# Optimization experiments

Measured on AMD Instinct MI355X. Metric: run time of the kernel, lower is better.

The kernel has to match this reference:

```python
import jax, jax.numpy as jnp
import numpy as np

# GeoFormer.generate_proposal constants (cfg.threshold_ins, cfg.min_pts_num,
# instance classes start at semantic id 4 on ScanNet)
THRESHOLD = 0.5
MIN_PTS_NUM = 50
MIN_INST_CLASS = 4


def setup_inputs() -> dict:
    key = jax.random.key(0)
    k1, k2, k3, k4 = jax.random.split(key, 4)
    B, Q, N, C = 4, 128, 50000, 20
    mask_logits = jax.random.normal(k1, (B, Q, N), dtype=jnp.float32)
    cls_logits = jax.random.normal(k2, (B, Q, C), dtype=jnp.float32)
    seg_pred = jax.random.randint(k3, (B, N), 0, C, dtype=jnp.int64)
    fg_idxs = jax.random.randint(k4, (B * N,), 0, 300000, dtype=jnp.int64)
    return {"mask_logits": mask_logits, "cls_logits": cls_logits,
            "seg_pred": seg_pred, "fg_idxs": fg_idxs}


def reference(mask_logits, cls_logits, seg_pred, fg_idxs):
    # mask_logits: [B, Q, N]  per-query point-mask logits (dense form of the
    #   per-batch list in the original; batch_offsets become the B dim)
    # cls_logits:  [B, Q, C]  per-query class logits
    # seg_pred:    [B, N]     per-point semantic prediction
    # fg_idxs:     [B*N]      foreground -> original point id map
    B, Q, N = mask_logits.shape
    m = jax.nn.sigmoid(mask_logits)                         # [B, Q, N]
    cls_pred = jnp.argmax(cls_logits, axis=2)               # [B, Q]

    # (mask_logit_b[n] > threshold) & (seg_pred == cls_logits_pred[b, n])
    sel = (m > THRESHOLD) & (seg_pred[:, None, :] == cls_pred[:, :, None])  # [B,Q,N]
    cnt = sel.sum(axis=-1)                                  # [B, Q] proposal sizes

    # score = mean of sigmoid over selected points
    msel = jnp.where(sel, m, jnp.zeros((), m.dtype))
    scores = msel.sum(axis=-1) / jnp.maximum(cnt, 1).astype(m.dtype)  # [B, Q]

    # skip if too few points or a background/wall class (< 4)
    valid = (cnt >= MIN_PTS_NUM) & (cls_pred >= MIN_INST_CLASS)       # [B, Q]

    proposal_masks = sel & valid[:, :, None]                # dense proposal_idx
    scores = jnp.where(valid, scores, jnp.zeros((), scores.dtype))
    global_ids = fg_idxs.reshape(B, N)                      # fg_idxs remap per point
    return proposal_masks, scores, valid, cls_pred, global_ids
```

## Files before the change

kernel.cpp:

```cpp
#include <hip/hip_runtime.h>
#include <math.h>

#define BB 4
#define QQ 128
#define NN 50000
#define CC 20
#define ROWS (BB * QQ)
#define NV4 (NN / 4)
#define TPB 256
#define UNROLL 4
#define BPR 13
#define THRESH_CNT 50
#define MIN_CLS 4

typedef float f32x4 __attribute__((ext_vector_type(4)));
typedef int   i32x4 __attribute__((ext_vector_type(4)));

struct Ws {
    float sum[ROWS];
    int   cnt[ROWS];
    int   cls[ROWS];
    int   valid[ROWS];
};

__global__ void k0_argmax_zero(const float* __restrict__ cls_logits, Ws* ws) {
    int r = blockIdx.x * blockDim.x + threadIdx.x;
    if (r >= ROWS) return;
    const float* p = cls_logits + r * CC;
    float best = p[0];
    int bi = 0;
    #pragma unroll
    for (int c = 1; c < CC; ++c) {
        float v = p[c];
        if (v > best) { best = v; bi = c; }
    }
    ws->cls[r] = bi;
    ws->sum[r] = 0.0f;
    ws->cnt[r] = 0;
}

__global__ __launch_bounds__(256) void k1_select(
        const float* __restrict__ mask_logits,
        const int*   __restrict__ seg_pred,
        float* __restrict__ out_mask,
        Ws* __restrict__ ws) {
    const int row = blockIdx.y;
    const int b   = row >> 7;
    const int cls = ws->cls[row];

    const f32x4* __restrict__ ml = (const f32x4*)(mask_logits + (size_t)row * NN);
    const i32x4* __restrict__ sp = (const i32x4*)(seg_pred + b * NN);
    f32x4* __restrict__ om = (f32x4*)(out_mask + (size_t)row * NN);

    const int idx0 = blockIdx.x * (TPB * UNROLL) + threadIdx.x;

    f32x4 v[UNROLL];
    i32x4 s[UNROLL];
    bool  act[UNROLL];
    #pragma unroll
    for (int j = 0; j < UNROLL; ++j) {
        int idx = idx0 + j * TPB;
        act[j] = (idx < NV4);
        if (act[j]) {
            v[j] = ml[idx];
            s[j] = sp[idx];
        }
    }

    float lsum = 0.0f;
    int   lcnt = 0;
    #pragma unroll
    for (int j = 0; j < UNROLL; ++j) {
        if (!act[j]) continue;
        int idx = idx0 + j * TPB;
        f32x4 vv = v[j];
        i32x4 ss = s[j];
        bool s0 = (vv.x > 0.0f) & (ss.x == cls);
        bool s1 = (vv.y > 0.0f) & (ss.y == cls);
        bool s2 = (vv.z > 0.0f) & (ss.z == cls);
        bool s3 = (vv.w > 0.0f) & (ss.w == cls);
        float g0 = 1.0f / (1.0f + __expf(-vv.x));
        float g1 = 1.0f / (1.0f + __expf(-vv.y));
        float g2 = 1.0f / (1.0f + __expf(-vv.z));
        float g3 = 1.0f / (1.0f + __expf(-vv.w));
        f32x4 o;
        o.x = s0 ? 1.0f : 0.0f;
        o.y = s1 ? 1.0f : 0.0f;
        o.z = s2 ? 1.0f : 0.0f;
        o.w = s3 ? 1.0f : 0.0f;
        lsum += (s0 ? g0 : 0.0f) + (s1 ? g1 : 0.0f)
              + (s2 ? g2 : 0.0f) + (s3 ? g3 : 0.0f);
        lcnt += (int)s0 + (int)s1 + (int)s2 + (int)s3;
        __builtin_nontemporal_store(o, &om[idx]);
    }

    #pragma unroll
    for (int off = 32; off > 0; off >>= 1) {
        lsum += __shfl_down(lsum, off);
        lcnt += __shfl_down(lcnt, off);
    }
    __shared__ float ssum[4];
    __shared__ int   scnt[4];
    const int wave = threadIdx.x >> 6;
    const int lane = threadIdx.x & 63;
    if (lane == 0) { ssum[wave] = lsum; scnt[wave] = lcnt; }
    __syncthreads();
    if (threadIdx.x == 0) {
        float ts = ssum[0] + ssum[1] + ssum[2] + ssum[3];
        int   tc = scnt[0] + scnt[1] + scnt[2] + scnt[3];
        atomicAdd(&ws->sum[row], ts);
        atomicAdd(&ws->cnt[row], tc);
    }
}

__global__ void k2_finalize_gids(const int* __restrict__ fg,
                                 float* __restrict__ out,
                                 Ws* __restrict__ ws) {
    const int idx = blockIdx.x * blockDim.x + threadIdx.x;
    if (idx < ROWS) {
        int   cnt = ws->cnt[idx];
        int   cls = ws->cls[idx];
        float sum = ws->sum[idx];
        int valid = (cnt >= THRESH_CNT) && (cls >= MIN_CLS);
        ws->valid[idx] = valid;
        float* tail = out + (size_t)ROWS * NN;
        tail[idx]            = valid ? (sum / (float)max(cnt, 1)) : 0.0f;
        tail[ROWS + idx]     = valid ? 1.0f : 0.0f;
        tail[2 * ROWS + idx] = (float)cls;
    }
    const int nv4 = (BB * NN) / 4;
    if (idx < nv4) {
        float* gids = out + (size_t)ROWS * NN + 3 * ROWS;
        i32x4 v = ((const i32x4*)fg)[idx];
        f32x4 o;
        o.x = (float)v.x; o.y = (float)v.y; o.z = (float)v.z; o.w = (float)v.w;
        __builtin_nontemporal_store(o, &((f32x4*)gids)[idx]);
    }
}

__global__ __launch_bounds__(256) void k3_fixup(
        float* __restrict__ out_mask, const Ws* __restrict__ ws) {
    const int row = blockIdx.y;
    if (ws->valid[row]) return;
    f32x4* __restrict__ om = (f32x4*)(out_mask + (size_t)row * NN);
    const f32x4 z = {0.0f, 0.0f, 0.0f, 0.0f};
    const int idx0 = blockIdx.x * (TPB * UNROLL) + threadIdx.x;
    #pragma unroll
    for (int j = 0; j < UNROLL; ++j) {
        int idx = idx0 + j * TPB;
        if (idx < NV4) __builtin_nontemporal_store(z, &om[idx]);
    }
}

extern "C" void kernel_launch(void* const* d_in, const int* in_sizes, int n_in,
                              void* d_out, int out_size, void* d_ws, size_t ws_size,
                              hipStream_t stream) {
    const float* mask_logits = (const float*)d_in[0];
    const float* cls_logits  = (const float*)d_in[1];
    const int*   seg_pred    = (const int*)d_in[2];
    const int*   fg_idxs     = (const int*)d_in[3];

    float* out = (float*)d_out;
    Ws* ws = (Ws*)d_ws;

    float* out_mask = out;

    k0_argmax_zero<<<(ROWS + 255) / 256, 256, 0, stream>>>(cls_logits, ws);

    dim3 g1(BPR, ROWS);
    k1_select<<<g1, TPB, 0, stream>>>(mask_logits, seg_pred, out_mask, ws);

    const int gids_blocks = ((BB * NN) / 4 + 255) / 256;
    k2_finalize_gids<<<gids_blocks, 256, 0, stream>>>(fg_idxs, out, ws);

    k3_fixup<<<g1, TPB, 0, stream>>>(out_mask, ws);
}
```

Baseline: 197.8 us.

## Give each block a larger contiguous chunk with software-pipelined batched loads

Reduces blocks per row from 13 to 4. Each block now handles a contiguous quarter of the row (3125 float4s) as three batches of four loads plus a tail. The next batch is prefetched while the current one is computed, to hide memory latency and cut per-block launch and atomic overhead. The cost is fewer blocks in flight (2048 instead of 6656) and higher register pressure, which may lower occupancy for a bandwidth-bound kernel. The fixup kernel is changed to match the new partitioning.

```diff
diff --git a/kernel.cpp b/kernel.cpp
--- a/kernel.cpp
+++ b/kernel.cpp
@@ -8,8 +8,10 @@
 #define ROWS (BB * QQ)
 #define NV4 (NN / 4)
 #define TPB 256
-#define UNROLL 4
-#define BPR 13
+#define BPR 4
+#define QUOTA (NV4 / BPR)
+#define FULL_ITERS 12
+#define TAIL 53
 #define THRESH_CNT 50
 #define MIN_CLS 4
 
@@ -47,57 +49,89 @@
     const int row = blockIdx.y;
     const int b   = row >> 7;
     const int cls = ws->cls[row];
-
-    const f32x4* __restrict__ ml = (const f32x4*)(mask_logits + (size_t)row * NN);
-    const i32x4* __restrict__ sp = (const i32x4*)(seg_pred + b * NN);
-    f32x4* __restrict__ om = (f32x4*)(out_mask + (size_t)row * NN);
-
-    const int idx0 = blockIdx.x * (TPB * UNROLL) + threadIdx.x;
-
-    f32x4 v[UNROLL];
-    i32x4 s[UNROLL];
-    bool  act[UNROLL];
-    #pragma unroll
-    for (int j = 0; j < UNROLL; ++j) {
-        int idx = idx0 + j * TPB;
-        act[j] = (idx < NV4);
-        if (act[j]) {
-            v[j] = ml[idx];
-            s[j] = sp[idx];
-        }
-    }
+    const int off = blockIdx.x * QUOTA;
+
+    const f32x4* __restrict__ ml = (const f32x4*)(mask_logits + (size_t)row * NN) + off;
+    const i32x4* __restrict__ sp = (const i32x4*)(seg_pred + b * NN) + off;
+    f32x4* __restrict__ om = (f32x4*)(out_mask + (size_t)row * NN) + off;
+
+    const int t = threadIdx.x;
 
     float lsum = 0.0f;
     int   lcnt = 0;
-    #pragma unroll
-    for (int j = 0; j < UNROLL; ++j) {
-        if (!act[j]) continue;
-        int idx = idx0 + j * TPB;
-        f32x4 vv = v[j];
-        i32x4 ss = s[j];
-        bool s0 = (vv.x > 0.0f) & (ss.x == cls);
-        bool s1 = (vv.y > 0.0f) & (ss.y == cls);
-        bool s2 = (vv.z > 0.0f) & (ss.z == cls);
-        bool s3 = (vv.w > 0.0f) & (ss.w == cls);
+
+    f32x4 v0[4]; i32x4 s0v[4];
+    #pragma unroll
+    for (int j = 0; j < 4; ++j) {
+        v0[j]  = ml[t + j * TPB];
+        s0v[j] = sp[t + j * TPB];
+    }
+
+    #pragma unroll
+    for (int bat = 0; bat < 3; ++bat) {
+        f32x4 nv[4]; i32x4 ns[4];
+        if (bat < 2) {
+            const int nbase = (bat + 1) * (4 * TPB) + t;
+            #pragma unroll
+            for (int j = 0; j < 4; ++j) {
+                nv[j] = ml[nbase + j * TPB];
+                ns[j] = sp[nbase + j * TPB];
+            }
+        }
+        const int base = bat * (4 * TPB) + t;
+        #pragma unroll
+        for (int j = 0; j < 4; ++j) {
+            f32x4 vv = v0[j];
+            i32x4 ss = s0v[j];
+            bool c0 = (vv.x > 0.0f) & (ss.x == cls);
+            bool c1 = (vv.y > 0.0f) & (ss.y == cls);
+            bool c2 = (vv.z > 0.0f) & (ss.z == cls);
+            bool c3 = (vv.w > 0.0f) & (ss.w == cls);
+            float g0 = 1.0f / (1.0f + __expf(-vv.x));
+            float g1 = 1.0f / (1.0f + __expf(-vv.y));
+            float g2 = 1.0f / (1.0f + __expf(-vv.z));
+            float g3 = 1.0f / (1.0f + __expf(-vv.w));
+            f32x4 o;
+            o.x = c0 ? 1.0f : 0.0f;
+            o.y = c1 ? 1.0f : 0.0f;
+            o.z = c2 ? 1.0f : 0.0f;
+            o.w = c3 ? 1.0f : 0.0f;
+            lsum += (c0 ? g0 : 0.0f) + (c1 ? g1 : 0.0f)
+                  + (c2 ? g2 : 0.0f) + (c3 ? g3 : 0.0f);
+            lcnt += (int)c0 + (int)c1 + (int)c2 + (int)c3;
+            __builtin_nontemporal_store(o, &om[base + j * TPB]);
+        }
+        #pragma unroll
+        for (int j = 0; j < 4; ++j) { v0[j] = nv[j]; s0v[j] = ns[j]; }
+    }
+
+    if (t < TAIL) {
+        const int idx = FULL_ITERS * TPB + t;
+        f32x4 vv = ml[idx];
+        i32x4 ss = sp[idx];
+        bool c0 = (vv.x > 0.0f) & (ss.x == cls);
+        bool c1 = (vv.y > 0.0f) & (ss.y == cls);
+        bool c2 = (vv.z > 0.0f) & (ss.z == cls);
+        bool c3 = (vv.w > 0.0f) & (ss.w == cls);
         float g0 = 1.0f / (1.0f + __expf(-vv.x));
         float g1 = 1.0f / (1.0f + __expf(-vv.y));
         float g2 = 1.0f / (1.0f + __expf(-vv.z));
         float g3 = 1.0f / (1.0f + __expf(-vv.w));
         f32x4 o;
-        o.x = s0 ? 1.0f : 0.0f;
-        o.y = s1 ? 1.0f : 0.0f;
-        o.z = s2 ? 1.0f : 0.0f;
-        o.w = s3 ? 1.0f : 0.0f;
-        lsum += (s0 ? g0 : 0.0f) + (s1 ? g1 : 0.0f)
-              + (s2 ? g2 : 0.0f) + (s3 ? g3 : 0.0f);
-        lcnt += (int)s0 + (int)s1 + (int)s2 + (int)s3;
+        o.x = c0 ? 1.0f : 0.0f;
+        o.y = c1 ? 1.0f : 0.0f;
+        o.z = c2 ? 1.0f : 0.0f;
+        o.w = c3 ? 1.0f : 0.0f;
+        lsum += (c0 ? g0 : 0.0f) + (c1 ? g1 : 0.0f)
+              + (c2 ? g2 : 0.0f) + (c3 ? g3 : 0.0f);
+        lcnt += (int)c0 + (int)c1 + (int)c2 + (int)c3;
         __builtin_nontemporal_store(o, &om[idx]);
     }
 
     #pragma unroll
-    for (int off = 32; off > 0; off >>= 1) {
-        lsum += __shfl_down(lsum, off);
-        lcnt += __shfl_down(lcnt, off);
+    for (int offr = 32; offr > 0; offr >>= 1) {
+        lsum += __shfl_down(lsum, offr);
+        lcnt += __shfl_down(lcnt, offr);
     }
     __shared__ float ssum[4];
     __shared__ int   scnt[4];
@@ -142,14 +176,15 @@
         float* __restrict__ out_mask, const Ws* __restrict__ ws) {
     const int row = blockIdx.y;
     if (ws->valid[row]) return;
-    f32x4* __restrict__ om = (f32x4*)(out_mask + (size_t)row * NN);
+    f32x4* __restrict__ om = (f32x4*)(out_mask + (size_t)row * NN)
+                             + blockIdx.x * QUOTA;
     const f32x4 z = {0.0f, 0.0f, 0.0f, 0.0f};
-    const int idx0 = blockIdx.x * (TPB * UNROLL) + threadIdx.x;
-    #pragma unroll
-    for (int j = 0; j < UNROLL; ++j) {
-        int idx = idx0 + j * TPB;
-        if (idx < NV4) __builtin_nontemporal_store(z, &om[idx]);
-    }
+    const int t = threadIdx.x;
+    #pragma unroll
+    for (int i = 0; i < FULL_ITERS; ++i)
+        __builtin_nontemporal_store(z, &om[t + i * TPB]);
+    if (t < TAIL)
+        __builtin_nontemporal_store(z, &om[FULL_ITERS * TPB + t]);
 }
 
 extern "C" void kernel_launch(void* const* d_in, const int* in_sizes, int n_in,
```

Result: slower. 204.4 us (+3.3%).
